# Kernel tuning notes

Hardware: AMD Instinct MI355X
Metric: run time of the kernel (lower is better)

Reference implementation:

```python
import jax, jax.numpy as jnp
import numpy as np

N = 50000      # nodes per graph (template.shape[1])
DIM = 3        # template.shape[0]
B = 32         # batch of graphs
E = 150000     # edges per graph
BN_EPS = 1e-5


def setup_inputs() -> dict:
    key = jax.random.key(0)
    ks = jax.random.split(key, 24)

    def w(k, shape):
        s = 1.0 / np.sqrt(shape[0])
        return jax.random.normal(k, shape, jnp.float32) * s

    H = 2 * DIM
    inp = {
        "x": jax.random.normal(ks[0], (B * N, DIM), jnp.float32),
        "edge_base": jax.random.randint(ks[1], (2, E), 0, N, dtype=jnp.int32),
        "W1": w(ks[2], (DIM, H)), "b1": jnp.zeros((H,), jnp.float32),
        "g1": jnp.ones((H,), jnp.float32), "be1": jnp.zeros((H,), jnp.float32),
        "W2": w(ks[3], (H, H)), "b2": jnp.zeros((H,), jnp.float32),
        "g2": jnp.ones((H,), jnp.float32), "be2": jnp.zeros((H,), jnp.float32),
        "W3": w(ks[4], (H, H)), "b3": jnp.zeros((H,), jnp.float32),
        "g3": jnp.ones((H,), jnp.float32), "be3": jnp.zeros((H,), jnp.float32),
        "lw1": w(ks[5], (N * H, 256)), "lb1": jnp.zeros((256,), jnp.float32),
        "lw2": w(ks[6], (256, 128)), "lb2": jnp.zeros((128,), jnp.float32),
        "lw3": w(ks[7], (128, 64)), "lb3": jnp.zeros((64,), jnp.float32),
        "lw4": w(ks[8], (64, 32)), "lb4": jnp.zeros((32,), jnp.float32),
        "num_graphs": B,
        "num_nodes": N,
    }
    return inp


def _gcn_norm(edge_base, num_graphs, num_nodes):
    """Batched edge index with self-loops + symmetric GCN normalization."""
    NB = num_graphs * num_nodes
    offsets = (jnp.arange(num_graphs, dtype=jnp.int32) * num_nodes)
    # replicate per-graph edges with node-id offset: [2, B*E]
    ei = (edge_base[:, None, :] + offsets[None, :, None]).reshape(2, -1)
    loop = jnp.arange(NB, dtype=jnp.int32)
    row = jnp.concatenate([ei[0], loop])  # source
    col = jnp.concatenate([ei[1], loop])  # target
    deg = jax.ops.segment_sum(jnp.ones_like(col, jnp.float32), col, num_segments=NB)
    dis = jnp.where(deg > 0, jax.lax.rsqrt(jnp.maximum(deg, 1.0)), 0.0)
    norm = dis[row] * dis[col]
    return row, col, norm, NB


def _gcn_conv(h, row, col, norm, NB, W, b):
    m = h @ W                               # transform then propagate (PyG GCNConv)
    msg = m[row] * norm[:, None]            # gather + scale
    agg = jax.ops.segment_sum(msg, col, num_segments=NB)  # scatter-add
    return agg + b


def _bn(o, g, be):
    mu = o.mean(axis=0)
    var = o.var(axis=0)
    return g * (o - mu) * jax.lax.rsqrt(var + BN_EPS) + be


def reference(x, edge_base, W1, b1, g1, be1, W2, b2, g2, be2, W3, b3, g3, be3,
              lw1, lb1, lw2, lb2, lw3, lb3, lw4, lb4, num_graphs, num_nodes):
    row, col, norm, NB = _gcn_norm(edge_base, num_graphs, num_nodes)
    o = jax.nn.relu(_bn(_gcn_conv(x, row, col, norm, NB, W1, b1), g1, be1))
    o = jax.nn.relu(_bn(_gcn_conv(o, row, col, norm, NB, W2, b2), g2, be2))
    o = jax.nn.relu(_bn(_gcn_conv(o, row, col, norm, NB, W3, b3), g3, be3))
    o = o.reshape(num_graphs, -1)           # [B, N*2*dim]
    o = jax.nn.relu(o @ lw1 + lb1)
    o = jax.nn.relu(o @ lw2 + lb2)
    o = jax.nn.relu(o @ lw3 + lb3)
    return o @ lw4 + lb4                    # [B, 32]
```

## Files before the change

### kernel.cpp

```cpp
#include <hip/hip_runtime.h>

#define NNODES 50000
#define BGR 32
#define ROWF 192
#define BN_EPS 1e-5f
#define NC 50
#define GSPLITS (NNODES / NC)
#define RGROUPS 16
#define GATHER_BLOCKS 1024

__global__ void count_deg_kernel(const int* __restrict__ col, int E, int* __restrict__ deg) {
    int e = blockIdx.x * blockDim.x + threadIdx.x;
    if (e < E) atomicAdd(&deg[col[e]], 1);
}

__global__ void make_dis_kernel(const int* __restrict__ deg, float* __restrict__ dis, int N) {
    int n = blockIdx.x * blockDim.x + threadIdx.x;
    if (n < N) dis[n] = rsqrtf((float)(deg[n] + 1));
}

__global__ __launch_bounds__(256) void scanA_kernel(const int* __restrict__ deg, int* __restrict__ bsum, int N) {
    __shared__ int lds[256];
    int i = blockIdx.x * 256 + threadIdx.x;
    lds[threadIdx.x] = (i < N) ? deg[i] : 0;
    __syncthreads();
    for (int off = 128; off > 0; off >>= 1) {
        if (threadIdx.x < off) lds[threadIdx.x] += lds[threadIdx.x + off];
        __syncthreads();
    }
    if (threadIdx.x == 0) bsum[blockIdx.x] = lds[0];
}

__global__ __launch_bounds__(256) void scanB_kernel(const int* __restrict__ bsum, int* __restrict__ bbase,
                                                    int* __restrict__ offsN, int nblk) {
    __shared__ int lds[256];
    int t = threadIdx.x;
    int v = (t < nblk) ? bsum[t] : 0;
    lds[t] = v;
    __syncthreads();
    for (int off = 1; off < 256; off <<= 1) {
        int u = (t >= off) ? lds[t - off] : 0;
        __syncthreads();
        lds[t] += u;
        __syncthreads();
    }
    if (t < nblk) bbase[t] = lds[t] - v;
    if (t == 255) offsN[0] = lds[255];
}

__global__ __launch_bounds__(256) void scanC_kernel(const int* __restrict__ deg, const int* __restrict__ bbase,
                                                    int* __restrict__ offs, int* __restrict__ cursor, int N) {
    __shared__ int lds[256];
    int i = blockIdx.x * 256 + threadIdx.x;
    int t = threadIdx.x;
    int v = (i < N) ? deg[i] : 0;
    lds[t] = v;
    __syncthreads();
    for (int off = 1; off < 256; off <<= 1) {
        int u = (t >= off) ? lds[t - off] : 0;
        __syncthreads();
        lds[t] += u;
        __syncthreads();
    }
    if (i < N) {
        int excl = bbase[blockIdx.x] + lds[t] - v;
        offs[i] = excl;
        cursor[i] = excl;
    }
}

__global__ void fill_csr_kernel(const int* __restrict__ row, const int* __restrict__ col,
                                const float* __restrict__ dis, int* __restrict__ cursor,
                                int2* __restrict__ csr_rw, int E) {
    int e = blockIdx.x * blockDim.x + threadIdx.x;
    if (e >= E) return;
    int r = row[e], c = col[e];
    int pos = atomicAdd(&cursor[c], 1);
    csr_rw[pos] = make_int2(r, __float_as_int(dis[r] * dis[c]));
}

__global__ __launch_bounds__(256) void t1_kernel(const float* __restrict__ x,
                                                 const float* __restrict__ W,
                                                 float* __restrict__ m, int N) {
    __shared__ float xt[BGR][ROWF];
    __shared__ float sW[18];
    int tid = threadIdx.x;
    if (tid < 18) sW[tid] = W[tid];
    int n0 = blockIdx.x * 64;
    int nval = N - n0; if (nval > 64) nval = 64;
    int lim = nval * 3;
    for (int b = 0; b < BGR; b++) {
        if (tid < lim) xt[b][tid] = x[((size_t)b * N + n0) * 3 + tid];
    }
    __syncthreads();
    for (int i = 0; i < 8; i++) {
        int pi = i * 256 + tid;
        int nl = pi >> 5, b = pi & 31;
        if (nl < nval) {
            float h0 = xt[b][nl * 3], h1 = xt[b][nl * 3 + 1], h2 = xt[b][nl * 3 + 2];
            float* mp = m + (size_t)(n0 + nl) * ROWF + b * 6;
            #pragma unroll
            for (int j = 0; j < 6; j++)
                mp[j] = h0 * sW[j] + h1 * sW[6 + j] + h2 * sW[12 + j];
        }
    }
}

__global__ __launch_bounds__(256) void t23_kernel(float* buf,
                                                  const float* __restrict__ stats,
                                                  const float* __restrict__ gam,
                                                  const float* __restrict__ bet,
                                                  const float* __restrict__ W, int NB) {
    __shared__ float sW[36];
    int tid = threadIdx.x;
    if (tid < 36) sW[tid] = W[tid];
    __syncthreads();
    float inv = 1.f / (float)NB;
    float sa[6], sc[6];
    #pragma unroll
    for (int j = 0; j < 6; j++) {
        float mu = stats[j] * inv;
        float var = stats[6 + j] * inv - mu * mu;
        float rs = rsqrtf(var + BN_EPS);
        float a = gam[j] * rs;
        sa[j] = a; sc[j] = bet[j] - mu * a;
    }
    size_t i = (size_t)blockIdx.x * 256 + tid;
    if (i >= (size_t)NB) return;
    float* p = buf + i * 6;
    float2 a0 = *(float2*)p, a1 = *(float2*)(p + 2), a2 = *(float2*)(p + 4);
    float h[6] = {a0.x, a0.y, a1.x, a1.y, a2.x, a2.y};
    #pragma unroll
    for (int k = 0; k < 6; k++) {
        float v = fmaf(sa[k], h[k], sc[k]);
        h[k] = v > 0.f ? v : 0.f;
    }
    float o[6];
    #pragma unroll
    for (int j = 0; j < 6; j++) {
        float t = 0.f;
        #pragma unroll
        for (int k = 0; k < 6; k++) t = fmaf(h[k], sW[k * 6 + j], t);
        o[j] = t;
    }
    *(float2*)p = make_float2(o[0], o[1]);
    *(float2*)(p + 2) = make_float2(o[2], o[3]);
    *(float2*)(p + 4) = make_float2(o[4], o[5]);
}

__global__ __launch_bounds__(256) void gather_kernel(const float* __restrict__ m,
                                                     const int* __restrict__ offs,
                                                     const int2* __restrict__ csr_rw,
                                                     const float* __restrict__ dis,
                                                     float* __restrict__ agg,
                                                     float* __restrict__ stats_out, int N) {
    int tid = threadIdx.x;
    int wv = tid >> 6, lane = tid & 63;
    bool lact = lane < 48;
    float4 ssum = make_float4(0.f, 0.f, 0.f, 0.f);
    float4 ssq  = make_float4(0.f, 0.f, 0.f, 0.f);
    int ngrp = (N + 3) >> 2;
    for (int grp = blockIdx.x; grp < ngrp; grp += gridDim.x) {
        int n = grp * 4 + wv;
        if (n >= N) continue;
        float4 acc = make_float4(0.f, 0.f, 0.f, 0.f);
        float d = dis[n];
        int s = offs[n], e = offs[n + 1];
        int r = n;
        float w0 = d * d;
        for (int p = s; ; p++) {
            int2 rwn = make_int2(0, 0);
            if (p < e) rwn = csr_rw[p];
            if (lact) {
                const float4 v = *(const float4*)(m + (size_t)r * ROWF + lane * 4);
                acc.x = fmaf(w0, v.x, acc.x);
                acc.y = fmaf(w0, v.y, acc.y);
                acc.z = fmaf(w0, v.z, acc.z);
                acc.w = fmaf(w0, v.w, acc.w);
            }
            if (p >= e) break;
            r = rwn.x;
            w0 = __int_as_float(rwn.y);
        }
        if (lact) *(float4*)(agg + (size_t)n * ROWF + lane * 4) = acc;
        ssum.x += acc.x; ssum.y += acc.y; ssum.z += acc.z; ssum.w += acc.w;
        ssq.x = fmaf(acc.x, acc.x, ssq.x); ssq.y = fmaf(acc.y, acc.y, ssq.y);
        ssq.z = fmaf(acc.z, acc.z, ssq.z); ssq.w = fmaf(acc.w, acc.w, ssq.w);
    }
    float vals[8] = {ssum.x, ssum.y, ssum.z, ssum.w, ssq.x, ssq.y, ssq.z, ssq.w};
    #pragma unroll
    for (int q = 0; q < 8; q++) {
        vals[q] += __shfl_down(vals[q], 24, 64);
        vals[q] += __shfl_down(vals[q], 12, 64);
        vals[q] += __shfl_down(vals[q], 6, 64);
        vals[q] += __shfl_down(vals[q], 3, 64);
    }
    __shared__ float red[4][3][8];
    if (lane < 3) {
        #pragma unroll
        for (int q = 0; q < 8; q++) red[wv][lane][q] = vals[q];
    }
    __syncthreads();
    if (tid < 24) {
        int l0 = tid >> 3, qq = tid & 7;
        float v = red[0][l0][qq] + red[1][l0][qq] + red[2][l0][qq] + red[3][l0][qq];
        int j = (4 * l0 + (qq & 3)) % 6;
        atomicAdd(&stats_out[(qq < 4 ? 0 : 6) + j], v);
    }
}

__global__ __launch_bounds__(256) void gemm1_kernel(const float* __restrict__ agg3,
                                                    const float* __restrict__ stats,
                                                    const float* __restrict__ gam,
                                                    const float* __restrict__ bet,
                                                    const float* __restrict__ lw1,
                                                    float* __restrict__ partials, int NB) {
    __shared__ float s_act[NC * ROWF];
    int tid = threadIdx.x;
    float inv = 1.f / (float)NB;
    float sa[6], sc[6];
    #pragma unroll
    for (int j = 0; j < 6; j++) {
        float mu = stats[j] * inv;
        float var = stats[6 + j] * inv - mu * mu;
        float rs = rsqrtf(var + BN_EPS);
        float a = gam[j] * rs;
        sa[j] = a; sc[j] = bet[j] - mu * a;
    }
    int n0 = blockIdx.x * NC;
    for (int idx = tid; idx < NC * ROWF; idx += 256) {
        float v = agg3[(size_t)n0 * ROWF + idx];
        int j = idx % 6;
        float t = fmaf(sa[j], v, sc[j]);
        s_act[idx] = t > 0.f ? t : 0.f;
    }
    __syncthreads();
    int wv = tid >> 6, lane = tid & 63;
    int b0 = wv * 8;
    float4 acc[8];
    #pragma unroll
    for (int i = 0; i < 8; i++) acc[i] = make_float4(0.f, 0.f, 0.f, 0.f);
    const float* wbase = lw1 + (size_t)n0 * 6 * 256 + 4 * lane;
    for (int nl = 0; nl < NC; nl++) {
        float4 w6[6];
        #pragma unroll
        for (int j = 0; j < 6; j++)
            w6[j] = *(const float4*)(wbase + ((size_t)nl * 6 + j) * 256);
        const float* hb = &s_act[nl * ROWF + b0 * 6];
        #pragma unroll
        for (int bb = 0; bb < 8; bb++) {
            const float* hp = hb + bb * 6;
            float2 h01 = *(const float2*)hp;
            float2 h23 = *(const float2*)(hp + 2);
            float2 h45 = *(const float2*)(hp + 4);
            float4 a = acc[bb];
            a.x = fmaf(h01.x, w6[0].x, a.x); a.y = fmaf(h01.x, w6[0].y, a.y);
            a.z = fmaf(h01.x, w6[0].z, a.z); a.w = fmaf(h01.x, w6[0].w, a.w);
            a.x = fmaf(h01.y, w6[1].x, a.x); a.y = fmaf(h01.y, w6[1].y, a.y);
            a.z = fmaf(h01.y, w6[1].z, a.z); a.w = fmaf(h01.y, w6[1].w, a.w);
            a.x = fmaf(h23.x, w6[2].x, a.x); a.y = fmaf(h23.x, w6[2].y, a.y);
            a.z = fmaf(h23.x, w6[2].z, a.z); a.w = fmaf(h23.x, w6[2].w, a.w);
            a.x = fmaf(h23.y, w6[3].x, a.x); a.y = fmaf(h23.y, w6[3].y, a.y);
            a.z = fmaf(h23.y, w6[3].z, a.z); a.w = fmaf(h23.y, w6[3].w, a.w);
            a.x = fmaf(h45.x, w6[4].x, a.x); a.y = fmaf(h45.x, w6[4].y, a.y);
            a.z = fmaf(h45.x, w6[4].z, a.z); a.w = fmaf(h45.x, w6[4].w, a.w);
            a.x = fmaf(h45.y, w6[5].x, a.x); a.y = fmaf(h45.y, w6[5].y, a.y);
            a.z = fmaf(h45.y, w6[5].z, a.z); a.w = fmaf(h45.y, w6[5].w, a.w);
            acc[bb] = a;
        }
    }
    #pragma unroll
    for (int bb = 0; bb < 8; bb++)
        *(float4*)&partials[(((size_t)blockIdx.x * BGR) + b0 + bb) * 256 + 4 * lane] = acc[bb];
}

__global__ __launch_bounds__(256) void reduce1_kernel(const float* __restrict__ partials,
                                                      float* __restrict__ p2) {
    int o = blockIdx.x * 256 + threadIdx.x;
    int g = blockIdx.y;
    float a = 0.f;
    for (int s = g; s < GSPLITS; s += RGROUPS)
        a += partials[(size_t)s * (BGR * 256) + o];
    p2[g * (BGR * 256) + o] = a;
}

__global__ __launch_bounds__(1024) void tail_kernel(const float* __restrict__ p2,
                                                    const float* __restrict__ lb1,
                                                    const float* __restrict__ lw2, const float* __restrict__ lb2,
                                                    const float* __restrict__ lw3, const float* __restrict__ lb3,
                                                    const float* __restrict__ lw4, const float* __restrict__ lb4,
                                                    float* __restrict__ out) {
    __shared__ float red[4][256];
    __shared__ float s1[256], s2[128], s3[64];
    int b = blockIdx.x;
    int tid = threadIdx.x;
    int c = tid & 255, sg = tid >> 8;
    float a = 0.f;
    for (int g = sg; g < RGROUPS; g += 4)
        a += p2[g * (BGR * 256) + b * 256 + c];
    red[sg][c] = a;
    __syncthreads();
    if (tid < 256) {
        float v = red[0][tid] + red[1][tid] + red[2][tid] + red[3][tid] + lb1[tid];
        s1[tid] = v > 0.f ? v : 0.f;
    }
    __syncthreads();
    if (tid < 128) {
        float acc = lb2[tid];
        for (int k = 0; k < 256; k++) acc += s1[k] * lw2[k * 128 + tid];
        s2[tid] = acc > 0.f ? acc : 0.f;
    }
    __syncthreads();
    if (tid < 64) {
        float acc = lb3[tid];
        for (int k = 0; k < 128; k++) acc += s2[k] * lw3[k * 64 + tid];
        s3[tid] = acc > 0.f ? acc : 0.f;
    }
    __syncthreads();
    if (tid < 32) {
        float acc = lb4[tid];
        for (int k = 0; k < 64; k++) acc += s3[k] * lw4[k * 32 + tid];
        out[b * 32 + tid] = acc;
    }
}

extern "C" void kernel_launch(void* const* d_in, const int* in_sizes, int n_in,
                              void* d_out, int out_size, void* d_ws, size_t ws_size,
                              hipStream_t stream) {
    const float* x   = (const float*)d_in[0];
    const int* edge  = (const int*)d_in[1];
    const float* W1  = (const float*)d_in[2];
    const float* g1  = (const float*)d_in[4];
    const float* be1 = (const float*)d_in[5];
    const float* W2  = (const float*)d_in[6];
    const float* g2  = (const float*)d_in[8];
    const float* be2 = (const float*)d_in[9];
    const float* W3  = (const float*)d_in[10];
    const float* g3  = (const float*)d_in[12];
    const float* be3 = (const float*)d_in[13];
    const float* lw1 = (const float*)d_in[14];
    const float* lb1 = (const float*)d_in[15];
    const float* lw2 = (const float*)d_in[16];
    const float* lb2 = (const float*)d_in[17];
    const float* lw3 = (const float*)d_in[18];
    const float* lb3 = (const float*)d_in[19];
    const float* lw4 = (const float*)d_in[20];
    const float* lb4 = (const float*)d_in[21];

    const int E = in_sizes[1] / 2;
    const int N = NNODES;
    const int B = in_sizes[0] / (N * 3);
    const int NB = B * N;
    const int nblk = (N + 255) / 256;

    char* ws = (char*)d_ws;
    size_t bufBytes = (size_t)N * ROWF * sizeof(float);
    float* buf0 = (float*)ws;
    float* buf1 = (float*)(ws + bufBytes);
    char* p = ws + 2 * bufBytes;
    float* dis    = (float*)p;  p += (size_t)N * 4;
    int*   deg    = (int*)p;    p += (size_t)N * 4;
    int*   offs   = (int*)p;    p += (size_t)(N + 1) * 4;
    int*   cursor = (int*)p;    p += (size_t)N * 4;
    int*   bsum   = (int*)p;    p += 256 * 4;
    int*   bbase  = (int*)p;    p += 256 * 4;
    int2*  csr_rw = (int2*)p;   p += (size_t)E * 8;
    float* stats  = (float*)p;  p += 48 * 4;
    float* p2     = (float*)p;  p += (size_t)RGROUPS * BGR * 256 * 4;
    float* stats1 = stats, *stats2 = stats + 16, *stats3 = stats + 32;
    float* partials = buf0;

    const int T = 256;

    hipMemsetAsync(deg, 0, (size_t)N * 4, stream);
    hipMemsetAsync(stats, 0, 48 * 4, stream);
    count_deg_kernel<<<(E + T - 1) / T, T, 0, stream>>>(edge + E, E, deg);
    make_dis_kernel<<<(N + T - 1) / T, T, 0, stream>>>(deg, dis, N);
    scanA_kernel<<<nblk, T, 0, stream>>>(deg, bsum, N);
    scanB_kernel<<<1, T, 0, stream>>>(bsum, bbase, offs + N, nblk);
    scanC_kernel<<<nblk, T, 0, stream>>>(deg, bbase, offs, cursor, N);
    fill_csr_kernel<<<(E + T - 1) / T, T, 0, stream>>>(edge, edge + E, dis, cursor, csr_rw, E);

    t1_kernel<<<(N + 63) / 64, T, 0, stream>>>(x, W1, buf0, N);
    gather_kernel<<<GATHER_BLOCKS, T, 0, stream>>>(buf0, offs, csr_rw, dis, buf1, stats1, N);
    t23_kernel<<<(NB + T - 1) / T, T, 0, stream>>>(buf1, stats1, g1, be1, W2, NB);
    gather_kernel<<<GATHER_BLOCKS, T, 0, stream>>>(buf1, offs, csr_rw, dis, buf0, stats2, N);
    t23_kernel<<<(NB + T - 1) / T, T, 0, stream>>>(buf0, stats2, g2, be2, W3, NB);
    gather_kernel<<<GATHER_BLOCKS, T, 0, stream>>>(buf0, offs, csr_rw, dis, buf1, stats3, N);

    gemm1_kernel<<<GSPLITS, T, 0, stream>>>(buf1, stats3, g3, be3, lw1, partials, NB);
    reduce1_kernel<<<dim3(32, RGROUPS), T, 0, stream>>>(partials, p2);
    tail_kernel<<<B, 1024, 0, stream>>>(p2, lb1, lw2, lb2, lw3, lb3, lw4, lb4, (float*)d_out);
}
```

Measured before the change: 465.1 us.

## Unroll CSR gather by two with dual accumulators, nontemporal lw1 loads

The gather loop now handles two CSR edges per iteration with independent accumulators, so two row loads are in flight at once instead of a serial dependent chain. The self-loop term is hoisted out of the loop. Gather grid size is doubled. In the first linear layer, weight loads use nontemporal hints and the node loop is unrolled by two to stream the large lw1 matrix without polluting cache. This trades extra register use for more memory-level parallelism.

Measured after the change: 619.5 us. +33.2%, slower.

```diff
diff --git a/kernel.cpp b/kernel.cpp
--- a/kernel.cpp
+++ b/kernel.cpp
@@ -7,7 +7,9 @@
 #define NC 50
 #define GSPLITS (NNODES / NC)
 #define RGROUPS 16
-#define GATHER_BLOCKS 1024
+#define GATHER_BLOCKS 2048
+
+typedef float __attribute__((ext_vector_type(4))) f32x4;
 
 __global__ void count_deg_kernel(const int* __restrict__ col, int E, int* __restrict__ deg) {
     int e = blockIdx.x * blockDim.x + threadIdx.x;
@@ -157,32 +159,49 @@
     int tid = threadIdx.x;
     int wv = tid >> 6, lane = tid & 63;
     bool lact = lane < 48;
+    int loff = lane * 4;
     float4 ssum = make_float4(0.f, 0.f, 0.f, 0.f);
     float4 ssq  = make_float4(0.f, 0.f, 0.f, 0.f);
     int ngrp = (N + 3) >> 2;
     for (int grp = blockIdx.x; grp < ngrp; grp += gridDim.x) {
         int n = grp * 4 + wv;
         if (n >= N) continue;
-        float4 acc = make_float4(0.f, 0.f, 0.f, 0.f);
         float d = dis[n];
         int s = offs[n], e = offs[n + 1];
-        int r = n;
-        float w0 = d * d;
-        for (int p = s; ; p++) {
-            int2 rwn = make_int2(0, 0);
-            if (p < e) rwn = csr_rw[p];
+        float4 acc0 = make_float4(0.f, 0.f, 0.f, 0.f);
+        float4 acc1 = make_float4(0.f, 0.f, 0.f, 0.f);
+        if (lact) {
+            const float4 v = *(const float4*)(m + (size_t)n * ROWF + loff);
+            float w = d * d;
+            acc0.x = w * v.x; acc0.y = w * v.y; acc0.z = w * v.z; acc0.w = w * v.w;
+        }
+        int p = s;
+        for (; p + 1 < e; p += 2) {
+            int2 e0 = csr_rw[p];
+            int2 e1 = csr_rw[p + 1];
             if (lact) {
-                const float4 v = *(const float4*)(m + (size_t)r * ROWF + lane * 4);
-                acc.x = fmaf(w0, v.x, acc.x);
-                acc.y = fmaf(w0, v.y, acc.y);
-                acc.z = fmaf(w0, v.z, acc.z);
-                acc.w = fmaf(w0, v.w, acc.w);
+                const float4 v0 = *(const float4*)(m + (size_t)e0.x * ROWF + loff);
+                const float4 v1 = *(const float4*)(m + (size_t)e1.x * ROWF + loff);
+                float w0 = __int_as_float(e0.y), w1 = __int_as_float(e1.y);
+                acc0.x = fmaf(w0, v0.x, acc0.x); acc0.y = fmaf(w0, v0.y, acc0.y);
+                acc0.z = fmaf(w0, v0.z, acc0.z); acc0.w = fmaf(w0, v0.w, acc0.w);
+                acc1.x = fmaf(w1, v1.x, acc1.x); acc1.y = fmaf(w1, v1.y, acc1.y);
+                acc1.z = fmaf(w1, v1.z, acc1.z); acc1.w = fmaf(w1, v1.w, acc1.w);
             }
-            if (p >= e) break;
-            r = rwn.x;
-            w0 = __int_as_float(rwn.y);
         }
-        if (lact) *(float4*)(agg + (size_t)n * ROWF + lane * 4) = acc;
+        if (p < e) {
+            int2 e0 = csr_rw[p];
+            if (lact) {
+                const float4 v0 = *(const float4*)(m + (size_t)e0.x * ROWF + loff);
+                float w0 = __int_as_float(e0.y);
+                acc0.x = fmaf(w0, v0.x, acc0.x); acc0.y = fmaf(w0, v0.y, acc0.y);
+                acc0.z = fmaf(w0, v0.z, acc0.z); acc0.w = fmaf(w0, v0.w, acc0.w);
+            }
+        }
+        float4 acc;
+        acc.x = acc0.x + acc1.x; acc.y = acc0.y + acc1.y;
+        acc.z = acc0.z + acc1.z; acc.w = acc0.w + acc1.w;
+        if (lact) *(float4*)(agg + (size_t)n * ROWF + loff) = acc;
         ssum.x += acc.x; ssum.y += acc.y; ssum.z += acc.z; ssum.w += acc.w;
         ssq.x = fmaf(acc.x, acc.x, ssq.x); ssq.y = fmaf(acc.y, acc.y, ssq.y);
         ssq.z = fmaf(acc.z, acc.z, ssq.z); ssq.w = fmaf(acc.w, acc.w, ssq.w);
@@ -241,11 +260,12 @@
     #pragma unroll
     for (int i = 0; i < 8; i++) acc[i] = make_float4(0.f, 0.f, 0.f, 0.f);
     const float* wbase = lw1 + (size_t)n0 * 6 * 256 + 4 * lane;
+    #pragma unroll 2
     for (int nl = 0; nl < NC; nl++) {
-        float4 w6[6];
+        f32x4 w6[6];
         #pragma unroll
         for (int j = 0; j < 6; j++)
-            w6[j] = *(const float4*)(wbase + ((size_t)nl * 6 + j) * 256);
+            w6[j] = __builtin_nontemporal_load((const f32x4*)(wbase + ((size_t)nl * 6 + j) * 256));
         const float* hb = &s_act[nl * ROWF + b0 * 6];
         #pragma unroll
         for (int bb = 0; bb < 8; bb++) {
```
